# Optimization experiments

Hardware: AMD Instinct MI355X
Metric: run time of the kernel (lower is better)

Reference implementation:

```python
import jax, jax.numpy as jnp
import numpy as np

_L, _DEPTH, _M, _NGEN, _C = 4, 7, 256, 8, 16


def _build_tree():
    # Complete _L-ary tree in BFS (level) order. t columns: [label, parent, position, child_0.._L-1]
    rng = np.random.default_rng(0)
    sizes = [_L ** d for d in range(_DEPTH + 1)]
    t_limits = np.concatenate([[0], np.cumsum(sizes)]).astype(np.int32)
    n = int(t_limits[-1])
    u = np.arange(n)
    parent = np.where(u > 0, (u - 1) // _L, 0)
    pos = np.where(u > 0, (u - 1) % _L, 0)
    labels = rng.integers(0, _M, n)
    ch = _L * u[:, None] + 1 + np.arange(_L)[None, :]
    ch = np.where(ch < n, ch, 0)  # 0 == no child (root is never a child)
    t = np.concatenate([labels[:, None], parent[:, None], pos[:, None], ch], axis=1).astype(np.int32)
    return t, t_limits


def setup_inputs():
    key = jax.random.key(0)
    ka, kb, kp = jax.random.split(key, 3)
    t, t_limits = _build_tree()
    return {
        'a': jax.random.normal(ka, (_NGEN, _C, _C, _L), jnp.float32),
        'b': jax.random.normal(kb, (_NGEN, _C, _M), jnp.float32),
        'pi': jax.random.normal(kp, (_NGEN, _C), jnp.float32),
        't': jnp.asarray(t),
        't_limits': jnp.asarray(t_limits),
    }


def _htmm_likelihood(a, b, pi, t, t_limits):
    t = np.asarray(t)
    lim = np.asarray(t_limits)
    n_levels = len(lim) - 1
    n = int(lim[-1])
    n_gen, C, _, L = a.shape
    sm_a = jax.nn.softmax(a, axis=1)    # [G, Ci(child), Cj(parent), L]
    sm_b = jax.nn.softmax(b, axis=2)    # [G, C, M]
    sm_pi = jax.nn.softmax(pi, axis=1)  # [G, C]

    # ---- preliminary downward: per-node state priors, level by level ----
    prior = jnp.zeros((n_gen, n, C), sm_pi.dtype).at[:, 0, :].set(sm_pi)
    for lev in range(1, n_levels):
        lo, hi = int(lim[lev]), int(lim[lev + 1])
        pos, pa = t[lo:hi, 2], t[lo:hi, 1]
        a_pos = sm_a[:, :, :, pos]                        # [G, Ci, Cj, nl]
        lev_prior = jnp.einsum('gijn,gnj->gni', a_pos, prior[:, pa, :])
        prior = prior.at[:, lo:hi, :].set(lev_prior)

    # ---- upward pass ----
    beta_i = jnp.zeros((n_gen, n, C), sm_pi.dtype)
    beta_il = jnp.zeros((n_gen, n + 1, C), sm_pi.dtype)   # extra dummy slot for padded children
    lo, hi = int(lim[-2]), int(lim[-1])                   # leaves
    em = sm_b[:, :, t[lo:hi, 0]].transpose(0, 2, 1)       # [G, n_leaf, C]
    bl = em * prior[:, lo:hi, :]
    beta_i = beta_i.at[:, lo:hi, :].set(bl / bl.sum(2, keepdims=True))
    a_t = sm_a.transpose(0, 3, 1, 2)                      # [G, L(pos), Ci, Cj]
    for lev in range(n_levels - 2, -1, -1):
        lo, hi = int(lim[lev]), int(lim[lev + 1])
        ch = t[lo:hi, 3:]                                 # [nl, L]
        mask = ch > 0
        safe = np.where(mask, ch, 0)
        ratio = beta_i[:, safe, :] / prior[:, safe, :]    # [G, nl, L, C]
        bil = jnp.einsum('gnlc,glcp->gnlp', ratio, a_t)   # [G, nl, L, Cj]
        aux = jnp.prod(jnp.where(mask[None, :, :, None], bil, 1.0), axis=2)
        em = sm_b[:, :, t[lo:hi, 0]].transpose(0, 2, 1)
        bi = aux * em * prior[:, lo:hi, :]
        beta_i = beta_i.at[:, lo:hi, :].set(bi / bi.sum(2, keepdims=True))
        scat = np.where(mask, ch, n).reshape(-1)          # padded children go to dummy slot
        beta_il = beta_il.at[:, scat, :].set(bil.reshape(n_gen, -1, C))
    beta_il = beta_il[:, :n, :].at[:, 0, :].set(0.0)

    # ---- downward pass: smoothed posteriors ----
    eps_i = jnp.zeros((n_gen, n, C), sm_pi.dtype).at[:, 0, :].set(beta_i[:, 0, :])
    eps_ijl = jnp.zeros((n_gen, n, C, C), sm_pi.dtype)
    for lev in range(1, n_levels):
        lo, hi = int(lim[lev]), int(lim[lev + 1])
        pos, pa = t[lo:hi, 2], t[lo:hi, 1]
        a_pos = sm_a[:, :, :, pos].transpose(0, 3, 1, 2)  # [G, nl, Ci, Cj]
        num = beta_i[:, lo:hi, :, None] * a_pos * eps_i[:, pa, None, :]
        den = prior[:, lo:hi, :, None] * beta_il[:, lo:hi, None, :]
        e_ijl = num / den
        e_i = e_ijl.sum(3)
        e_i = e_i / e_i.sum(2, keepdims=True)
        eps_i = eps_i.at[:, lo:hi, :].set(e_i)
        eps_ijl = eps_ijl.at[:, lo:hi, :, :].set(e_ijl)

    # ---- log-likelihood ----
    pi_lh = jnp.sum(eps_i[:, 0, :] * jnp.log(sm_pi), axis=-1)
    b_nodes = sm_b[:, :, t[:, 0]].transpose(0, 2, 1)      # [G, n, C]
    b_lh = jnp.sum(eps_i * jnp.log(b_nodes), axis=(1, 2))
    a_pos_all = sm_a[:, :, :, t[1:, 2]].transpose(0, 3, 1, 2)
    a_lh = jnp.sum(eps_ijl[:, 1:] * jnp.log(a_pos_all), axis=(1, 2, 3))
    return pi_lh + b_lh + a_lh  # [n_gen]


def reference(a, b, pi, t, t_limits):
    return _htmm_likelihood(a, b, pi, t, t_limits)
```

## Files before the change

kernel.cpp:

```cpp
#include <hip/hip_runtime.h>

#define NGEN 8
#define NC 16
#define NM 256
#define NNODE 21845

#define OFF_SMA_T  ((size_t)0)
#define OFF_SALA   ((size_t)8192)
#define OFF_SMA_U  ((size_t)16384)
#define OFF_SMB_T  ((size_t)24576)
#define OFF_LSMB_T ((size_t)57344)
#define OFF_SMPI   ((size_t)90112)
#define OFF_LSMPI  ((size_t)90240)
#define OFF_LAB    ((size_t)90368)
#define OFF_R4     ((size_t)112224)
#define OFF_EPS4   ((size_t)144992)

__device__ __forceinline__ float red16(float v) {
    v += __shfl_xor(v, 1, 16);
    v += __shfl_xor(v, 2, 16);
    v += __shfl_xor(v, 4, 16);
    v += __shfl_xor(v, 8, 16);
    return v;
}
__device__ __forceinline__ float rcpf(float x) { return __builtin_amdgcn_rcpf(x); }

__device__ __forceinline__ float dot16(const float* A, const float* row) {
    const float4* r4 = (const float4*)row;
    float s = 0.f;
#pragma unroll
    for (int q = 0; q < 4; ++q) {
        float4 t = r4[q];
        s += A[4 * q] * t.x + A[4 * q + 1] * t.y + A[4 * q + 2] * t.z + A[4 * q + 3] * t.w;
    }
    return s;
}
__device__ __forceinline__ void dot16x2(const float* A, const float* B, const float* row,
                                        float& s1, float& s2) {
    const float4* r4 = (const float4*)row;
#pragma unroll
    for (int q = 0; q < 4; ++q) {
        float4 t = r4[q];
        s1 += A[4 * q] * t.x + A[4 * q + 1] * t.y + A[4 * q + 2] * t.z + A[4 * q + 3] * t.w;
        s2 += B[4 * q] * t.x + B[4 * q + 1] * t.y + B[4 * q + 2] * t.z + B[4 * q + 3] * t.w;
    }
}

template <bool STORE_BIL>
__device__ __forceinline__ void up_step4(const float (*Rch)[16], float (*BILch)[16],
                                         const float (*Ppar)[16], float (*Rpar)[16],
                                         const float* smb, int lab, int nd, int l, int p,
                                         const float* Aup) {
    int ch = 4 * nd + l;
    float bil = dot16(Aup, Rch[ch]);
    if (STORE_BIL) BILch[ch][p] = bil;
    float t0 = bil * __shfl_xor(bil, 16);
    float aux = t0 * __shfl_xor(t0, 32);
    float q0 = aux * smb[(size_t)lab * 16 + p];
    float bi = q0 * Ppar[nd][p];
    float ssum = red16(bi);
    if (l == 0) Rpar[nd][p] = q0 * rcpf(ssum);
}

__global__ __launch_bounds__(256) void k_init(const float* __restrict__ a,
                                              const float* __restrict__ b,
                                              const float* __restrict__ pi,
                                              const int* __restrict__ t,
                                              float* __restrict__ ws, float* __restrict__ out) {
    int bx = blockIdx.x, tid = threadIdx.x;
    if (bx < 128) {
        int gtid = bx * 256 + tid;
        if (gtid < NNODE) ((int*)(ws + OFF_LAB))[gtid] = t[gtid * 7];
        int g = bx >> 4, i = bx & 15, m = tid;
        float v = b[((size_t)(g * NC + i)) * NM + m];
        __shared__ float sred[256];
        sred[m] = v;
        __syncthreads();
        for (int s = 128; s > 0; s >>= 1) { if (m < s) sred[m] = fmaxf(sred[m], sred[m + s]); __syncthreads(); }
        float mx = sred[0];
        __syncthreads();
        float ex = expf(v - mx);
        sred[m] = ex;
        __syncthreads();
        for (int s = 128; s > 0; s >>= 1) { if (m < s) sred[m] += sred[m + s]; __syncthreads(); }
        float sum = sred[0];
        ws[OFF_SMB_T + ((size_t)g * NM + m) * NC + i] = ex / sum;
        ws[OFF_LSMB_T + ((size_t)g * NM + m) * NC + i] = v - mx - logf(sum);
        return;
    }
    int g = bx - 128;
    if (tid < 64) {
        int j = tid >> 2, l = tid & 3;
        size_t base = ((size_t)(g * NC) * NC + j) * 4 + l;
        float v[16];
        float mx = -1e30f;
#pragma unroll
        for (int i = 0; i < 16; ++i) { v[i] = a[base + (size_t)i * 64]; mx = fmaxf(mx, v[i]); }
        float e[16], s = 0.0f;
#pragma unroll
        for (int i = 0; i < 16; ++i) { e[i] = expf(v[i] - mx); s += e[i]; }
        float ls = logf(s), rs = 1.0f / s;
        size_t tb = ((size_t)(g * NC + j) * 4 + l) * NC;
#pragma unroll
        for (int i = 0; i < 16; ++i) {
            float sm = e[i] * rs;
            float lg = v[i] - mx - ls;
            ws[OFF_SMA_T + tb + i] = sm;
            ws[OFF_SALA + tb + i] = sm * lg;
            ws[OFF_SMA_U + ((size_t)(g * NC + i) * 4 + l) * NC + j] = sm;
        }
    } else if (tid == 64) {
        float v[16];
        float mx = -1e30f;
#pragma unroll
        for (int i = 0; i < 16; ++i) { v[i] = pi[g * NC + i]; mx = fmaxf(mx, v[i]); }
        float e[16], s = 0.0f;
#pragma unroll
        for (int i = 0; i < 16; ++i) { e[i] = expf(v[i] - mx); s += e[i]; }
        float ls = logf(s), rs = 1.0f / s;
#pragma unroll
        for (int i = 0; i < 16; ++i) {
            ws[OFF_SMPI + g * NC + i] = e[i] * rs;
            ws[OFF_LSMPI + g * NC + i] = v[i] - mx - ls;
        }
        out[g] = 0.0f;
    }
}

__global__ __launch_bounds__(256) void k_sub_up(float* __restrict__ ws) {
    int s = blockIdx.x, g = blockIdx.y, tid = threadIdx.x;
    int v = 85 + s;
    int i = tid & 15, grp = tid >> 4, pos = grp & 3;
    int lane = tid & 63, wv = tid >> 6;
    int l = lane >> 4, p = lane & 15;
    const float* sAg = ws + OFF_SMA_T + (size_t)g * 1024;
    const float* Aug = ws + OFF_SMA_U + (size_t)g * 1024;
    const float* smb = ws + OFF_SMB_T + (size_t)g * 4096;
    const int* LAB = (const int*)(ws + OFF_LAB);

    __shared__ __align__(16) float P5[4][16], P6[16][16];
    __shared__ __align__(16) float R5[4][16], R6[16][16], R7[64][16];
    __shared__ __align__(16) float P4[16];
    __shared__ int labs[85];

    if (tid < 64) labs[21 + tid] = LAB[64 * v + 21 + tid];
    else if (tid < 80) labs[5 + (tid - 64)] = LAB[16 * v + 5 + (tid - 64)];
    else if (tid < 84) labs[1 + (tid - 80)] = LAB[4 * v + 1 + (tid - 80)];
    else if (tid == 84) labs[0] = LAB[v];
    else if (tid >= 128 && tid < 144) {
        int v3 = (v - 1) >> 2, v2 = (v3 - 1) >> 2, v1 = (v2 - 1) >> 2;
        int chain[4] = {v1, v2, v3, v};
        float pr = ws[OFF_SMPI + g * 16 + i];
#pragma unroll
        for (int k = 0; k < 4; ++k) {
            int pk = (chain[k] - 1) & 3;
            float sacc = 0.f;
#pragma unroll
            for (int j = 0; j < 16; ++j) sacc += sAg[(j * 4 + pk) * 16 + i] * __shfl(pr, j, 16);
            pr = sacc;
        }
        P4[i] = pr;
    }
    float Areg[16];
#pragma unroll
    for (int j = 0; j < 16; ++j) Areg[j] = sAg[(j * 4 + pos) * 16 + i];
    __syncthreads();

    if (tid < 64) P5[grp][i] = dot16(Areg, P4);
    __syncthreads();
    P6[grp][i] = dot16(Areg, P5[grp >> 2]);
    __syncthreads();
#pragma unroll
    for (int k = 0; k < 4; ++k) {
        int nl = grp + 16 * k;
        float s7 = dot16(Areg, P6[nl >> 2]);
        float smbv = smb[(size_t)labs[21 + nl] * 16 + i];
        float bl = smbv * s7;
        float ssum = red16(bl);
        R7[nl][i] = smbv * rcpf(ssum);
    }
    __syncthreads();
    float Aup[16];
#pragma unroll
    for (int c = 0; c < 16; ++c) Aup[c] = Aug[(c * 4 + l) * 16 + p];
#pragma unroll
    for (int r = 0; r < 4; ++r)
        up_step4<false>(R7, nullptr, P6, R6, smb, labs[5 + (wv + 4 * r)], wv + 4 * r, l, p, Aup);
    __syncthreads();
    up_step4<false>(R6, nullptr, P5, R5, smb, labs[1 + wv], wv, l, p, Aup);
    __syncthreads();
    if (wv == 0) {
        float bil = dot16(Aup, R5[l]);
        float t0 = bil * __shfl_xor(bil, 16);
        float aux = t0 * __shfl_xor(t0, 32);
        float q0 = aux * smb[(size_t)labs[0] * 16 + p];
        float bi = q0 * P4[p];
        float ssum = red16(bi);
        if (l == 0) ws[OFF_R4 + ((size_t)g * 256 + s) * 16 + p] = q0 * rcpf(ssum);
    }
}

__global__ __launch_bounds__(1024) void k_top(float* __restrict__ ws, float* __restrict__ out) {
    int g = blockIdx.x, tid = threadIdx.x;
    int i = tid & 15, grp = tid >> 4, pos = grp & 3;
    int lane = tid & 63, wv = tid >> 6;
    int l = lane >> 4, p = lane & 15;
    const float* sAg = ws + OFF_SMA_T + (size_t)g * 1024;
    const float* sLg = ws + OFF_SALA + (size_t)g * 1024;
    const float* Aug = ws + OFF_SMA_U + (size_t)g * 1024;
    const float* smb = ws + OFF_SMB_T + (size_t)g * 4096;
    const float* lsmb = ws + OFF_LSMB_T + (size_t)g * 4096;
    const float* r4g = ws + OFF_R4 + (size_t)g * 4096;
    float* eps4 = ws + OFF_EPS4 + (size_t)g * 4096;
    const int* LAB = (const int*)(ws + OFF_LAB);

    __shared__ float Pt[85][16], Bt[85][16], BILt[341][16];
    __shared__ int labt[341];
    __shared__ float wsum[16];

    float Areg[16], Aup[16], sLreg[16];
#pragma unroll
    for (int j = 0; j < 16; ++j) {
        Areg[j] = sAg[(j * 4 + pos) * 16 + i];
        sLreg[j] = sLg[(j * 4 + pos) * 16 + i];
    }
#pragma unroll
    for (int c = 0; c < 16; ++c) Aup[c] = Aug[(c * 4 + l) * 16 + p];
    if (tid < 341) labt[tid] = LAB[tid];
    if (tid < 16) Pt[0][i] = ws[OFF_SMPI + g * 16 + i];
    __syncthreads();
    if (grp < 4) {
        float pv = Pt[0][i];
        float s = 0.f;
#pragma unroll
        for (int j = 0; j < 16; ++j) s += Areg[j] * __shfl(pv, j, 16);
        Pt[1 + grp][i] = s;
    }
    __syncthreads();
    if (grp < 16) {
        float pv = Pt[1 + (grp >> 2)][i];
        float s = 0.f;
#pragma unroll
        for (int j = 0; j < 16; ++j) s += Areg[j] * __shfl(pv, j, 16);
        Pt[5 + grp][i] = s;
    }
    __syncthreads();
    {
        float pv = Pt[5 + (grp >> 2)][i];
        float s = 0.f;
#pragma unroll
        for (int j = 0; j < 16; ++j) s += Areg[j] * __shfl(pv, j, 16);
        Pt[21 + grp][i] = s;
    }
    __syncthreads();
    for (int r = 0; r < 4; ++r) {
        int nd = wv + 16 * r;
        int chl = 4 * nd + l;
        float rv = r4g[(size_t)chl * 16 + p];
        float bil = 0.f;
#pragma unroll
        for (int c = 0; c < 16; ++c) bil += __shfl(rv, c, 16) * Aup[c];
        BILt[85 + chl][p] = bil;
        float t0 = bil * __shfl_xor(bil, 16);
        float aux = t0 * __shfl_xor(t0, 32);
        float bi = aux * smb[(size_t)labt[21 + nd] * 16 + p] * Pt[21 + nd][p];
        float ssum = red16(bi);
        if (l == 0) Bt[21 + nd][p] = bi * rcpf(ssum);
    }
    __syncthreads();
    {
        int nd = wv, ch = 21 + 4 * nd + l;
        float rv = Bt[ch][p] * rcpf(Pt[ch][p]);
        float bil = 0.f;
#pragma unroll
        for (int c = 0; c < 16; ++c) bil += __shfl(rv, c, 16) * Aup[c];
        BILt[ch][p] = bil;
        float t0 = bil * __shfl_xor(bil, 16);
        float aux = t0 * __shfl_xor(t0, 32);
        float bi = aux * smb[(size_t)labt[5 + nd] * 16 + p] * Pt[5 + nd][p];
        float ssum = red16(bi);
        if (l == 0) Bt[5 + nd][p] = bi * rcpf(ssum);
    }
    __syncthreads();
    if (wv < 4) {
        int nd = wv, ch = 5 + 4 * nd + l;
        float rv = Bt[ch][p] * rcpf(Pt[ch][p]);
        float bil = 0.f;
#pragma unroll
        for (int c = 0; c < 16; ++c) bil += __shfl(rv, c, 16) * Aup[c];
        BILt[ch][p] = bil;
        float t0 = bil * __shfl_xor(bil, 16);
        float aux = t0 * __shfl_xor(t0, 32);
        float bi = aux * smb[(size_t)labt[1 + nd] * 16 + p] * Pt[1 + nd][p];
        float ssum = red16(bi);
        if (l == 0) Bt[1 + nd][p] = bi * rcpf(ssum);
    }
    __syncthreads();
    if (wv == 0) {
        int ch = 1 + l;
        float rv = Bt[ch][p] * rcpf(Pt[ch][p]);
        float bil = 0.f;
#pragma unroll
        for (int c = 0; c < 16; ++c) bil += __shfl(rv, c, 16) * Aup[c];
        BILt[ch][p] = bil;
        float t0 = bil * __shfl_xor(bil, 16);
        float aux = t0 * __shfl_xor(t0, 32);
        float bi = aux * smb[(size_t)labt[0] * 16 + p] * Pt[0][p];
        float ssum = red16(bi);
        if (l == 0) Bt[0][p] = bi * rcpf(ssum);
    }
    __syncthreads();
    float acc = 0.f;
    if (tid < 16)
        acc += Bt[0][i] * (ws[OFF_LSMPI + g * 16 + i] + lsmb[(size_t)labt[0] * 16 + i]);
    if (grp < 4) {
        int row = 1 + grp;
        float w = Bt[0][i] * rcpf(BILt[row][i]);
        float c0 = Bt[row][i] * rcpf(Pt[row][i]);
        float s1 = 0.f, s2 = 0.f;
#pragma unroll
        for (int j = 0; j < 16; ++j) { float wj = __shfl(w, j, 16); s1 += Areg[j] * wj; s2 += sLreg[j] * wj; }
        float esum = c0 * s1, tot = red16(esum), ev = esum * rcpf(tot);
        Bt[row][i] = ev;
        acc += c0 * s2 + ev * lsmb[(size_t)labt[row] * 16 + i];
    }
    __syncthreads();
    if (grp < 16) {
        int row = 5 + grp, pa = 1 + (grp >> 2);
        float w = Bt[pa][i] * rcpf(BILt[row][i]);
        float c0 = Bt[row][i] * rcpf(Pt[row][i]);
        float s1 = 0.f, s2 = 0.f;
#pragma unroll
        for (int j = 0; j < 16; ++j) { float wj = __shfl(w, j, 16); s1 += Areg[j] * wj; s2 += sLreg[j] * wj; }
        float esum = c0 * s1, tot = red16(esum), ev = esum * rcpf(tot);
        Bt[row][i] = ev;
        acc += c0 * s2 + ev * lsmb[(size_t)labt[row] * 16 + i];
    }
    __syncthreads();
    {
        int row = 21 + grp, pa = 5 + (grp >> 2);
        float w = Bt[pa][i] * rcpf(BILt[row][i]);
        float c0 = Bt[row][i] * rcpf(Pt[row][i]);
        float s1 = 0.f, s2 = 0.f;
#pragma unroll
        for (int j = 0; j < 16; ++j) { float wj = __shfl(w, j, 16); s1 += Areg[j] * wj; s2 += sLreg[j] * wj; }
        float esum = c0 * s1, tot = red16(esum), ev = esum * rcpf(tot);
        Bt[row][i] = ev;
        acc += c0 * s2 + ev * lsmb[(size_t)labt[row] * 16 + i];
    }
    __syncthreads();
    for (int k = 0; k < 4; ++k) {
        int nl = grp + 64 * k;
        int row = 85 + nl, pa = 21 + (nl >> 2);
        float w = Bt[pa][i] * rcpf(BILt[row][i]);
        float c0 = r4g[(size_t)nl * 16 + i];
        float s1 = 0.f, s2 = 0.f;
#pragma unroll
        for (int j = 0; j < 16; ++j) { float wj = __shfl(w, j, 16); s1 += Areg[j] * wj; s2 += sLreg[j] * wj; }
        float esum = c0 * s1, tot = red16(esum), ev = esum * rcpf(tot);
        eps4[(size_t)nl * 16 + i] = ev;
        acc += c0 * s2 + ev * lsmb[(size_t)labt[row] * 16 + i];
    }
#pragma unroll
    for (int o = 1; o < 64; o <<= 1) acc += __shfl_xor(acc, o);
    if ((tid & 63) == 0) wsum[tid >> 6] = acc;
    __syncthreads();
    if (tid == 0) {
        float stot = 0.f;
#pragma unroll
        for (int w2 = 0; w2 < 16; ++w2) stot += wsum[w2];
        atomicAdd(&out[g], stot);
    }
}

__global__ __launch_bounds__(256) void k_sub_down(float* __restrict__ ws, float* __restrict__ out) {
    int s = blockIdx.x, g = blockIdx.y, tid = threadIdx.x;
    int v = 85 + s;
    int i = tid & 15, grp = tid >> 4, pos = grp & 3;
    int lane = tid & 63, wv = tid >> 6;
    int l = lane >> 4, p = lane & 15;
    const float* sAg = ws + OFF_SMA_T + (size_t)g * 1024;
    const float* sLg = ws + OFF_SALA + (size_t)g * 1024;
    const float* Aug = ws + OFF_SMA_U + (size_t)g * 1024;
    const float* smb = ws + OFF_SMB_T + (size_t)g * 4096;
    const float* lsmb = ws + OFF_LSMB_T + (size_t)g * 4096;
    const int* LAB = (const int*)(ws + OFF_LAB);

    __shared__ __align__(16) float P5[4][16], P6[16][16];
    __shared__ __align__(16) float R5[4][16], R6[16][16], R7[64][16];
    __shared__ __align__(16) float BIL5[4][16], BIL6[16][16], BIL7[64][16];
    __shared__ __align__(16) float P4[16], E4[16];
    __shared__ int labs[85];
    __shared__ float wsum[4];

    if (tid < 64) labs[21 + tid] = LAB[64 * v + 21 + tid];
    else if (tid < 80) labs[5 + (tid - 64)] = LAB[16 * v + 5 + (tid - 64)];
    else if (tid < 84) labs[1 + (tid - 80)] = LAB[4 * v + 1 + (tid - 80)];
    else if (tid == 84) labs[0] = LAB[v];
    else if (tid >= 96 && tid < 112) E4[tid - 96] = ws[OFF_EPS4 + ((size_t)g * 256 + s) * 16 + (tid - 96)];
    else if (tid >= 128 && tid < 144) {
        int v3 = (v - 1) >> 2, v2 = (v3 - 1) >> 2, v1 = (v2 - 1) >> 2;
        int chain[4] = {v1, v2, v3, v};
        float pr = ws[OFF_SMPI + g * 16 + i];
#pragma unroll
        for (int k = 0; k < 4; ++k) {
            int pk = (chain[k] - 1) & 3;
            float sacc = 0.f;
#pragma unroll
            for (int j = 0; j < 16; ++j) sacc += sAg[(j * 4 + pk) * 16 + i] * __shfl(pr, j, 16);
            pr = sacc;
        }
        P4[i] = pr;
    }
    float Areg[16];
#pragma unroll
    for (int j = 0; j < 16; ++j) Areg[j] = sAg[(j * 4 + pos) * 16 + i];
    __syncthreads();

    if (tid < 64) P5[grp][i] = dot16(Areg, P4);
    __syncthreads();
    P6[grp][i] = dot16(Areg, P5[grp >> 2]);
    __syncthreads();
#pragma unroll
    for (int k = 0; k < 4; ++k) {
        int nl = grp + 16 * k;
        float s7 = dot16(Areg, P6[nl >> 2]);
        float smbv = smb[(size_t)labs[21 + nl] * 16 + i];
        float bl = smbv * s7;
        float ssum = red16(bl);
        R7[nl][i] = smbv * rcpf(ssum);
    }
    __syncthreads();
    float Aup[16];
#pragma unroll
    for (int c = 0; c < 16; ++c) Aup[c] = Aug[(c * 4 + l) * 16 + p];
#pragma unroll
    for (int r = 0; r < 4; ++r)
        up_step4<true>(R7, BIL7, P6, R6, smb, labs[5 + (wv + 4 * r)], wv + 4 * r, l, p, Aup);
    __syncthreads();
    up_step4<true>(R6, BIL6, P5, R5, smb, labs[1 + wv], wv, l, p, Aup);
    __syncthreads();
    if (wv == 0) BIL5[l][p] = dot16(Aup, R5[l]);
    float sLreg[16];
#pragma unroll
    for (int j = 0; j < 16; ++j) sLreg[j] = sLg[(j * 4 + pos) * 16 + i];

    float acc = 0.f;
    if (tid < 64) {
        float w = E4[i] * rcpf(BIL5[grp][i]);
        BIL5[grp][i] = w;
        float c0 = R5[grp][i];
        float s1 = 0.f, s2 = 0.f;
        dot16x2(Areg, sLreg, BIL5[grp], s1, s2);
        float esum = c0 * s1, tot = red16(esum), ev = esum * rcpf(tot);
        R5[grp][i] = ev;
        acc += c0 * s2 + ev * lsmb[(size_t)labs[1 + grp] * 16 + i];
    }
    __syncthreads();
    {
        float w = R5[grp >> 2][i] * rcpf(BIL6[grp][i]);
        BIL6[grp][i] = w;
        float c0 = R6[grp][i];
        float s1 = 0.f, s2 = 0.f;
        dot16x2(Areg, sLreg, BIL6[grp], s1, s2);
        float esum = c0 * s1, tot = red16(esum), ev = esum * rcpf(tot);
        R6[grp][i] = ev;
        acc += c0 * s2 + ev * lsmb[(size_t)labs[5 + grp] * 16 + i];
    }
    __syncthreads();
#pragma unroll
    for (int k = 0; k < 4; ++k) {
        int nl = grp + 16 * k;
        float w = R6[nl >> 2][i] * rcpf(BIL7[nl][i]);
        BIL7[nl][i] = w;
        float c0 = R7[nl][i];
        float s1 = 0.f, s2 = 0.f;
        dot16x2(Areg, sLreg, BIL7[nl], s1, s2);
        float esum = c0 * s1, tot = red16(esum), ev = esum * rcpf(tot);
        acc += c0 * s2 + ev * lsmb[(size_t)labs[21 + nl] * 16 + i];
    }
#pragma unroll
    for (int o = 1; o < 64; o <<= 1) acc += __shfl_xor(acc, o);
    if ((tid & 63) == 0) wsum[tid >> 6] = acc;
    __syncthreads();
    if (tid == 0) atomicAdd(&out[g], wsum[0] + wsum[1] + wsum[2] + wsum[3]);
}

extern "C" void kernel_launch(void* const* d_in, const int* in_sizes, int n_in,
                              void* d_out, int out_size, void* d_ws, size_t ws_size,
                              hipStream_t stream) {
    const float* a = (const float*)d_in[0];
    const float* b = (const float*)d_in[1];
    const float* pi = (const float*)d_in[2];
    const int* t = (const int*)d_in[3];
    float* out = (float*)d_out;
    float* ws = (float*)d_ws;

    k_init<<<136, 256, 0, stream>>>(a, b, pi, t, ws, out);
    k_sub_up<<<dim3(256, NGEN), 256, 0, stream>>>(ws);
    k_top<<<NGEN, 1024, 0, stream>>>(ws, out);
    k_sub_down<<<dim3(256, NGEN), 256, 0, stream>>>(ws, out);
}
```

Baseline: 75.23 us.

## Stash subtree upward state in workspace instead of recomputing it in the down pass

```diff
diff --git a/kernel.cpp b/kernel.cpp
--- a/kernel.cpp
+++ b/kernel.cpp
@@ -15,6 +15,14 @@
 #define OFF_LAB    ((size_t)90368)
 #define OFF_R4     ((size_t)112224)
 #define OFF_EPS4   ((size_t)144992)
+#define OFF_ST     ((size_t)177760)
+#define ST_R7   0
+#define ST_R6   1024
+#define ST_R5   1280
+#define ST_BIL7 1344
+#define ST_BIL6 2368
+#define ST_BIL5 2624
+#define ST_SZ   2688
 
 __device__ __forceinline__ float red16(float v) {
     v += __shfl_xor(v, 1, 16);
@@ -46,14 +54,13 @@
     }
 }
 
-template <bool STORE_BIL>
 __device__ __forceinline__ void up_step4(const float (*Rch)[16], float (*BILch)[16],
                                          const float (*Ppar)[16], float (*Rpar)[16],
                                          const float* smb, int lab, int nd, int l, int p,
                                          const float* Aup) {
     int ch = 4 * nd + l;
     float bil = dot16(Aup, Rch[ch]);
-    if (STORE_BIL) BILch[ch][p] = bil;
+    BILch[ch][p] = bil;
     float t0 = bil * __shfl_xor(bil, 16);
     float aux = t0 * __shfl_xor(t0, 32);
     float q0 = aux * smb[(size_t)lab * 16 + p];
@@ -62,30 +69,39 @@
     if (l == 0) Rpar[nd][p] = q0 * rcpf(ssum);
 }
 
-__global__ __launch_bounds__(256) void k_init(const float* __restrict__ a,
+__global__ __launch_bounds__(128) void k_init(const float* __restrict__ a,
                                               const float* __restrict__ b,
                                               const float* __restrict__ pi,
                                               const int* __restrict__ t,
                                               float* __restrict__ ws, float* __restrict__ out) {
     int bx = blockIdx.x, tid = threadIdx.x;
     if (bx < 128) {
-        int gtid = bx * 256 + tid;
-        if (gtid < NNODE) ((int*)(ws + OFF_LAB))[gtid] = t[gtid * 7];
-        int g = bx >> 4, i = bx & 15, m = tid;
-        float v = b[((size_t)(g * NC + i)) * NM + m];
-        __shared__ float sred[256];
-        sred[m] = v;
-        __syncthreads();
-        for (int s = 128; s > 0; s >>= 1) { if (m < s) sred[m] = fmaxf(sred[m], sred[m + s]); __syncthreads(); }
-        float mx = sred[0];
-        __syncthreads();
-        float ex = expf(v - mx);
-        sred[m] = ex;
-        __syncthreads();
-        for (int s = 128; s > 0; s >>= 1) { if (m < s) sred[m] += sred[m + s]; __syncthreads(); }
-        float sum = sred[0];
-        ws[OFF_SMB_T + ((size_t)g * NM + m) * NC + i] = ex / sum;
-        ws[OFF_LSMB_T + ((size_t)g * NM + m) * NC + i] = v - mx - logf(sum);
+        for (int k = bx * 128 + tid; k < NNODE; k += 128 * 128)
+            ((int*)(ws + OFF_LAB))[k] = t[k * 7];
+        if (tid < 64) {
+            int g = bx >> 4, i = bx & 15;
+            float v[4];
+            float mx = -1e30f;
+#pragma unroll
+            for (int q = 0; q < 4; ++q) {
+                v[q] = b[((size_t)(g * NC + i)) * NM + tid + 64 * q];
+                mx = fmaxf(mx, v[q]);
+            }
+#pragma unroll
+            for (int o = 1; o < 64; o <<= 1) mx = fmaxf(mx, __shfl_xor(mx, o));
+            float e[4], s = 0.f;
+#pragma unroll
+            for (int q = 0; q < 4; ++q) { e[q] = expf(v[q] - mx); s += e[q]; }
+#pragma unroll
+            for (int o = 1; o < 64; o <<= 1) s += __shfl_xor(s, o);
+            float ls = logf(s), rs = 1.0f / s;
+#pragma unroll
+            for (int q = 0; q < 4; ++q) {
+                int m = tid + 64 * q;
+                ws[OFF_SMB_T + ((size_t)g * NM + m) * NC + i] = e[q] * rs;
+                ws[OFF_LSMB_T + ((size_t)g * NM + m) * NC + i] = v[q] - mx - ls;
+            }
+        }
         return;
     }
     int g = bx - 128;
@@ -138,8 +154,14 @@
     const float* smb = ws + OFF_SMB_T + (size_t)g * 4096;
     const int* LAB = (const int*)(ws + OFF_LAB);
 
+    __shared__ __align__(16) float ST[ST_SZ];
+    float (*R7)[16]   = (float(*)[16])(ST + ST_R7);
+    float (*R6)[16]   = (float(*)[16])(ST + ST_R6);
+    float (*R5)[16]   = (float(*)[16])(ST + ST_R5);
+    float (*BIL7)[16] = (float(*)[16])(ST + ST_BIL7);
+    float (*BIL6)[16] = (float(*)[16])(ST + ST_BIL6);
+    float (*BIL5)[16] = (float(*)[16])(ST + ST_BIL5);
     __shared__ __align__(16) float P5[4][16], P6[16][16];
-    __shared__ __align__(16) float R5[4][16], R6[16][16], R7[64][16];
     __shared__ __align__(16) float P4[16];
     __shared__ int labs[85];
 
@@ -185,12 +207,13 @@
     for (int c = 0; c < 16; ++c) Aup[c] = Aug[(c * 4 + l) * 16 + p];
 #pragma unroll
     for (int r = 0; r < 4; ++r)
-        up_step4<false>(R7, nullptr, P6, R6, smb, labs[5 + (wv + 4 * r)], wv + 4 * r, l, p, Aup);
-    __syncthreads();
-    up_step4<false>(R6, nullptr, P5, R5, smb, labs[1 + wv], wv, l, p, Aup);
+        up_step4(R7, BIL7, P6, R6, smb, labs[5 + (wv + 4 * r)], wv + 4 * r, l, p, Aup);
+    __syncthreads();
+    up_step4(R6, BIL6, P5, R5, smb, labs[1 + wv], wv, l, p, Aup);
     __syncthreads();
     if (wv == 0) {
         float bil = dot16(Aup, R5[l]);
+        BIL5[l][p] = bil;
         float t0 = bil * __shfl_xor(bil, 16);
         float aux = t0 * __shfl_xor(t0, 32);
         float q0 = aux * smb[(size_t)labs[0] * 16 + p];
@@ -198,6 +221,11 @@
         float ssum = red16(bi);
         if (l == 0) ws[OFF_R4 + ((size_t)g * 256 + s) * 16 + p] = q0 * rcpf(ssum);
     }
+    __syncthreads();
+    float* dst = ws + OFF_ST + (size_t)(g * 256 + s) * ST_SZ;
+#pragma unroll
+    for (int k = tid; k < ST_SZ / 4; k += 256)
+        ((float4*)dst)[k] = ((const float4*)ST)[k];
 }
 
 __global__ __launch_bounds__(1024) void k_top(float* __restrict__ ws, float* __restrict__ out) {
@@ -377,73 +405,39 @@
     int s = blockIdx.x, g = blockIdx.y, tid = threadIdx.x;
     int v = 85 + s;
     int i = tid & 15, grp = tid >> 4, pos = grp & 3;
-    int lane = tid & 63, wv = tid >> 6;
-    int l = lane >> 4, p = lane & 15;
     const float* sAg = ws + OFF_SMA_T + (size_t)g * 1024;
     const float* sLg = ws + OFF_SALA + (size_t)g * 1024;
-    const float* Aug = ws + OFF_SMA_U + (size_t)g * 1024;
-    const float* smb = ws + OFF_SMB_T + (size_t)g * 4096;
     const float* lsmb = ws + OFF_LSMB_T + (size_t)g * 4096;
     const int* LAB = (const int*)(ws + OFF_LAB);
 
-    __shared__ __align__(16) float P5[4][16], P6[16][16];
-    __shared__ __align__(16) float R5[4][16], R6[16][16], R7[64][16];
-    __shared__ __align__(16) float BIL5[4][16], BIL6[16][16], BIL7[64][16];
-    __shared__ __align__(16) float P4[16], E4[16];
+    __shared__ __align__(16) float ST[ST_SZ];
+    float (*R7)[16]   = (float(*)[16])(ST + ST_R7);
+    float (*R6)[16]   = (float(*)[16])(ST + ST_R6);
+    float (*R5)[16]   = (float(*)[16])(ST + ST_R5);
+    float (*BIL7)[16] = (float(*)[16])(ST + ST_BIL7);
+    float (*BIL6)[16] = (float(*)[16])(ST + ST_BIL6);
+    float (*BIL5)[16] = (float(*)[16])(ST + ST_BIL5);
+    __shared__ __align__(16) float E4[16];
     __shared__ int labs[85];
     __shared__ float wsum[4];
 
+    const float* src = ws + OFF_ST + (size_t)(g * 256 + s) * ST_SZ;
+#pragma unroll
+    for (int k = tid; k < ST_SZ / 4; k += 256)
+        ((float4*)ST)[k] = ((const float4*)src)[k];
     if (tid < 64) labs[21 + tid] = LAB[64 * v + 21 + tid];
     else if (tid < 80) labs[5 + (tid - 64)] = LAB[16 * v + 5 + (tid - 64)];
     else if (tid < 84) labs[1 + (tid - 80)] = LAB[4 * v + 1 + (tid - 80)];
     else if (tid == 84) labs[0] = LAB[v];
     else if (tid >= 96 && tid < 112) E4[tid - 96] = ws[OFF_EPS4 + ((size_t)g * 256 + s) * 16 + (tid - 96)];
-    else if (tid >= 128 && tid < 144) {
-        int v3 = (v - 1) >> 2, v2 = (v3 - 1) >> 2, v1 = (v2 - 1) >> 2;
-        int chain[4] = {v1, v2, v3, v};
-        float pr = ws[OFF_SMPI + g * 16 + i];
-#pragma unroll
-        for (int k = 0; k < 4; ++k) {
-            int pk = (chain[k] - 1) & 3;
-            float sacc = 0.f;
-#pragma unroll
-            for (int j = 0; j < 16; ++j) sacc += sAg[(j * 4 + pk) * 16 + i] * __shfl(pr, j, 16);
-            pr = sacc;
-        }
-        P4[i] = pr;
-    }
-    float Areg[16];
-#pragma unroll
-    for (int j = 0; j < 16; ++j) Areg[j] = sAg[(j * 4 + pos) * 16 + i];
-    __syncthreads();
-
-    if (tid < 64) P5[grp][i] = dot16(Areg, P4);
-    __syncthreads();
-    P6[grp][i] = dot16(Areg, P5[grp >> 2]);
-    __syncthreads();
-#pragma unroll
-    for (int k = 0; k < 4; ++k) {
-        int nl = grp + 16 * k;
-        float s7 = dot16(Areg, P6[nl >> 2]);
-        float smbv = smb[(size_t)labs[21 + nl] * 16 + i];
-        float bl = smbv * s7;
-        float ssum = red16(bl);
-        R7[nl][i] = smbv * rcpf(ssum);
-    }
-    __syncthreads();
-    float Aup[16];
-#pragma unroll
-    for (int c = 0; c < 16; ++c) Aup[c] = Aug[(c * 4 + l) * 16 + p];
-#pragma unroll
-    for (int r = 0; r < 4; ++r)
-        up_step4<true>(R7, BIL7, P6, R6, smb, labs[5 + (wv + 4 * r)], wv + 4 * r, l, p, Aup);
-    __syncthreads();
-    up_step4<true>(R6, BIL6, P5, R5, smb, labs[1 + wv], wv, l, p, Aup);
-    __syncthreads();
-    if (wv == 0) BIL5[l][p] = dot16(Aup, R5[l]);
-    float sLreg[16];
-#pragma unroll
-    for (int j = 0; j < 16; ++j) sLreg[j] = sLg[(j * 4 + pos) * 16 + i];
+
+    float Areg[16], sLreg[16];
+#pragma unroll
+    for (int j = 0; j < 16; ++j) {
+        Areg[j] = sAg[(j * 4 + pos) * 16 + i];
+        sLreg[j] = sLg[(j * 4 + pos) * 16 + i];
+    }
+    __syncthreads();
 
     float acc = 0.f;
     if (tid < 64) {
@@ -496,7 +490,7 @@
     float* out = (float*)d_out;
     float* ws = (float*)d_ws;
 
-    k_init<<<136, 256, 0, stream>>>(a, b, pi, t, ws, out);
+    k_init<<<136, 128, 0, stream>>>(a, b, pi, t, ws, out);
     k_sub_up<<<dim3(256, NGEN), 256, 0, stream>>>(ws);
     k_top<<<NGEN, 1024, 0, stream>>>(ws, out);
     k_sub_down<<<dim3(256, NGEN), 256, 0, stream>>>(ws, out);
```

New measurement: 76.08 us. About the same (+1.1%).
